# Kernel tuning notes

Hardware: AMD Instinct MI355X
Metric: run time of the kernel (lower is better)

Reference implementation:

```python
import jax, jax.numpy as jnp
import numpy as np

SQN = 3      # hardcoded recurrence depth
ATT_H = 256  # hardcoded attention hidden size
STRIDE = 16  # segment length (hardcoded expand(-1,16,-1))


def setup_inputs() -> dict:
    key = jax.random.key(0)
    ks = jax.random.split(key, 12)
    B, Cin, H, V = 64, 512, 512, 512

    def w(k, shape, fan_in):
        return jax.random.normal(k, shape, jnp.float32) / np.sqrt(fan_in).astype(np.float32)

    return {
        "visual_input": jax.random.normal(ks[0], (B, Cin, V), jnp.float32),
        "text_feature": jax.random.normal(ks[1], (B, H), jnp.float32),
        # weights stored [in, out] (transposed vs torch nn.Linear)
        "vis_conv_w": w(ks[2], (Cin, H), Cin),   # 1x1 Conv1d == linear over channels
        "vis_conv_b": jnp.zeros((H,), jnp.float32),
        "glob_w": w(ks[3], (SQN, H, H), H),      # 3 distinct global_emb linears
        "glob_b": jnp.zeros((SQN, H), jnp.float32),
        "guide_w": w(ks[4], (2 * H, H), 2 * H),
        "guide_b": jnp.zeros((H,), jnp.float32),
        "att1_w": w(ks[5], (H, ATT_H), H),
        "att1_b": jnp.zeros((ATT_H,), jnp.float32),
        "att2_w": w(ks[6], (H, ATT_H), H),
        "att2_b": jnp.zeros((ATT_H,), jnp.float32),
        "att3_w": w(ks[7], (ATT_H, 1), ATT_H),
        "att3_b": jnp.zeros((1,), jnp.float32),
        "out_conv_w": w(ks[8], (H, H), H),       # 1x1 Conv1d
        "out_conv_b": jnp.zeros((H,), jnp.float32),
        "text_w": w(ks[9], (H, H), H),
        "text_b": jnp.zeros((H,), jnp.float32),
    }


def reference(visual_input, text_feature, vis_conv_w, vis_conv_b, glob_w, glob_b,
              guide_w, guide_b, att1_w, att1_b, att2_w, att2_b, att3_w, att3_b,
              out_conv_w, out_conv_b, text_w, text_b):
    B, Cin, V = visual_input.shape
    H = vis_conv_w.shape[1]
    S = V // STRIDE  # number of segments

    # vis_conv (1x1) + relu: [B, H, V]
    vis_h = jax.nn.relu(jnp.einsum('bcv,ch->bhv', visual_input, vis_conv_w)
                        + vis_conv_b[None, :, None])
    # split into segments: [B, S, T=16, H]
    vis_seg = vis_h.reshape(B, H, S, STRIDE).transpose(0, 2, 3, 1)
    # AvgPool1d(kernel=stride) == per-segment mean: [B, S, H]
    avg_seg = vis_seg.mean(axis=2)
    # text projection: [B, H]
    text_att = text_feature @ text_w + text_b

    # precompute att_fn2(vis_seg): [B, S, T, ATT_H] (loop-invariant)
    att2_pre = jnp.einsum('bsth,ha->bsta', vis_seg, att2_w) + att2_b

    prev_se = jnp.zeros((B, S, H), vis_seg.dtype)
    se_list, att_list = [], []
    for m in range(SQN):  # fixed 3-step recurrence, distinct weights per step
        v_n = jnp.einsum('bsh,hk->bsk', avg_seg, glob_w[m]) + glob_b[m]
        # guide_emb (Linear+ReLU) followed by an outer relu == single relu
        g_n = jax.nn.relu(jnp.concatenate([v_n, prev_se], axis=-1) @ guide_w + guide_b)
        att = jnp.tanh((g_n @ att1_w + att1_b)[:, :, None, :] + att2_pre)  # [B,S,T,A]
        att = att @ att3_w + att3_b                                        # [B,S,T,1]
        att = jax.nn.softmax(att, axis=2)  # softmax over the 16 frames
        prev_se = jnp.sum(vis_seg * att, axis=2)  # [B, S, H]
        se_list.append(prev_se)
        att_list.append(att)

    vis_for_att = jnp.stack(se_list, axis=2)  # [B, S, 3, H]
    fuse_att = jax.nn.softmax(jnp.einsum('bsmh,bh->bsm', vis_for_att, text_att), axis=2)
    vis_new = jnp.einsum('bsmh,bsm->bsh', vis_for_att, fuse_att)  # [B, S, H]

    # vis_out_conv (1x1) + relu over stacked segments: [B, H, S]
    vis_out = jax.nn.relu(jnp.einsum('bsh,hk->bks', vis_new, out_conv_w)
                          + out_conv_b[None, :, None])
    att_out = jnp.concatenate(att_list, axis=3)  # [B, S, 16, 3]
    return vis_out, att_out
```

## Files before the change

### kernel.cpp

```cpp
#include <hip/hip_runtime.h>

#define B_   64
#define CIN_ 512
#define H_   512
#define V_   512
#define S_   32
#define T_   16
#define A_   256
#define SQN_ 3
#define BS_  2048

typedef float  f32x4  __attribute__((ext_vector_type(4)));
typedef float  f32x2  __attribute__((ext_vector_type(2)));
typedef short  short8 __attribute__((ext_vector_type(8)));
typedef short  short4v __attribute__((ext_vector_type(4)));
typedef unsigned int uint4v __attribute__((ext_vector_type(4)));

__device__ __forceinline__ unsigned short f2bf(float f) {
    union { float f; unsigned int u; } v; v.f = f;
    unsigned int u = v.u;
    unsigned int r = (u + 0x7fffu + ((u >> 16) & 1u)) >> 16;
    return (unsigned short)r;
}
__device__ __forceinline__ float bf2f(unsigned short h) {
    union { unsigned int u; float f; } v; v.u = ((unsigned int)h) << 16;
    return v.f;
}

__device__ __forceinline__ void gload16(const void* g, void* l) {
    __builtin_amdgcn_global_load_lds(
        (const __attribute__((address_space(1))) unsigned int*)g,
        (__attribute__((address_space(3))) unsigned int*)l,
        16, 0, 0);
}

__global__ __launch_bounds__(256) void prep_kernel(
    const float* __restrict__ visual, const float* __restrict__ vis_conv_w,
    const float* __restrict__ att2_w, const float* __restrict__ guide_w,
    const float* __restrict__ att1_w, const float* __restrict__ out_conv_w,
    const float* __restrict__ glob_w, const float* __restrict__ text_feature,
    const float* __restrict__ text_w, const float* __restrict__ text_b,
    const float* __restrict__ glob_b, const float* __restrict__ guide_b,
    unsigned short* __restrict__ visT, unsigned short* __restrict__ wT_visconv,
    unsigned short* __restrict__ wT_att2, unsigned short* __restrict__ wT_guide,
    unsigned short* __restrict__ wT_att1, unsigned short* __restrict__ wT_out,
    unsigned short* __restrict__ glob_bf, float* __restrict__ text_part,
    float* __restrict__ bcomb)
{
    __shared__ __align__(16) char smem[32768];
    const int id  = blockIdx.x;
    const int tid = threadIdx.x;

    if (id < 128) {
        const int nt = id & 7, kc = id >> 3;
        const int n0 = nt * 64, kbase = kc * 32;
        float* Ts = (float*)smem;
        float* Ws = (float*)smem + 64 * 33;
        {
            const int m = tid >> 2, kk = (tid & 3) * 8;
            #pragma unroll
            for (int c = 0; c < 8; c += 4)
                *(f32x4*)&Ts[m * 33 + kk + c] =
                    *(const f32x4*)&text_feature[m * 512 + kbase + kk + c];
            const int kr = tid >> 3, nn = (tid & 7) * 8;
            #pragma unroll
            for (int c = 0; c < 8; c += 4)
                *(f32x4*)&Ws[kr * 65 + nn + c] =
                    *(const f32x4*)&text_w[(long long)(kbase + kr) * 512 + n0 + nn + c];
        }
        __syncthreads();
        const int tm = (tid >> 4) * 4, tn = (tid & 15) * 4;
        float acc[4][4] = {};
        for (int k = 0; k < 32; k++) {
            float a[4], b2[4];
            #pragma unroll
            for (int i = 0; i < 4; i++) a[i] = Ts[(tm + i) * 33 + k];
            #pragma unroll
            for (int j = 0; j < 4; j++) b2[j] = Ws[k * 65 + tn + j];
            #pragma unroll
            for (int i = 0; i < 4; i++)
                #pragma unroll
                for (int j = 0; j < 4; j++) acc[i][j] += a[i] * b2[j];
        }
        #pragma unroll
        for (int i = 0; i < 4; i++)
            #pragma unroll
            for (int j = 0; j < 4; j++)
                text_part[kc * (64 * 512) + (tm + i) * 512 + n0 + tn + j] =
                    acc[i][j] + (kc == 0 ? text_b[n0 + tn + j] : 0.0f);
        return;
    }
    if (id < 131) {
        const int m = id - 128;
        const int j2 = tid * 2;
        float a0 = guide_b[j2], a1 = guide_b[j2 + 1];
        const float* gb = glob_b + m * 512;
        #pragma unroll 8
        for (int k = 0; k < 512; k++) {
            const float g = gb[k];
            f32x2 w = *(const f32x2*)&guide_w[(long long)k * 512 + j2];
            a0 += g * w[0];
            a1 += g * w[1];
        }
        f32x2 o = {a0, a1};
        *(f32x2*)&bcomb[m * 512 + j2] = o;
        return;
    }
    if (id < 227) {
        const int base = (id - 131) * 8192 + tid * 4;
        #pragma unroll
        for (int it = 0; it < 8; it++) {
            f32x4 v = *(const f32x4*)&glob_w[base + it * 1024];
            short4v o;
            #pragma unroll
            for (int c = 0; c < 4; c++) o[c] = (short)f2bf(v[c]);
            *(short4v*)&glob_bf[base + it * 1024] = o;
        }
        return;
    }

    if (id >= 547) {
        const int q = id - 547;
        const int b = q >> 5, tile = q & 31;
        const int k0 = (tile >> 2) << 6;
        const int v0 = (tile & 3) << 7;
        const float* src = visual + (long long)b * 262144;
        unsigned short* dst = visT + (long long)b * 262144;
        float* tl = (float*)smem;

        const int wave = tid >> 6, lane = tid & 63;
        #pragma unroll
        for (int i = 0; i < 8; i++) {
            const int r2 = wave * 16 + i * 2;
            gload16(&src[(long long)(k0 + r2 + (lane >> 5)) * 512 + v0 + (lane & 31) * 4],
                    &tl[r2 * 128]);
        }
        __syncthreads();

        const int kl = (tid & 7) * 8;
        const int vb = tid >> 3;
        #pragma unroll
        for (int jv = 0; jv < 4; jv++) {
            const int v = vb + jv * 32;
            short8 o;
            #pragma unroll
            for (int i = 0; i < 8; i++)
                o[i] = (short)f2bf(tl[(kl + i) * 128 + v]);
            *(short8*)&dst[(long long)(v0 + v) * 512 + k0 + kl] = o;
        }
        return;
    }

    const float* src; unsigned short* dst; int Kd, Nd, tile;
    if (id < 291)      { tile = id - 227; src = vis_conv_w; dst = wT_visconv; Kd = 512;  Nd = 512; }
    else if (id < 323) { tile = id - 291; src = att2_w;     dst = wT_att2;    Kd = 512;  Nd = 256; }
    else if (id < 451) { tile = id - 323; src = guide_w;    dst = wT_guide;   Kd = 1024; Nd = 512; }
    else if (id < 483) { tile = id - 451; src = att1_w;     dst = wT_att1;    Kd = 512;  Nd = 256; }
    else               { tile = id - 483; src = out_conv_w; dst = wT_out;     Kd = 512;  Nd = 512; }

    unsigned int* tl = (unsigned int*)smem;
    const int xw = Nd >> 6;
    const int n0 = (tile % xw) << 6, k0 = (tile / xw) << 6;
    {
        const int r = tid >> 4;
        const int c4 = (tid & 15) * 4;
        #pragma unroll
        for (int j = 0; j < 4; j++) {
            const int row = j * 16 + r;
            f32x4 v = *(const f32x4*)&src[(long long)(k0 + row) * Nd + n0 + c4];
            #pragma unroll
            for (int c2 = 0; c2 < 4; c2++)
                tl[row * 65 + c4 + c2] = f2bf(v[c2]);
        }
    }
    __syncthreads();
    {
        const int v = tid >> 2, cq = (tid & 3) * 16;
        short8 o0, o1;
        #pragma unroll
        for (int j = 0; j < 8; j++) o0[j] = (short)tl[(cq + j) * 65 + v];
        #pragma unroll
        for (int j = 0; j < 8; j++) o1[j] = (short)tl[(cq + 8 + j) * 65 + v];
        *(short8*)&dst[(long long)(n0 + v) * Kd + k0 + cq] = o0;
        *(short8*)&dst[(long long)(n0 + v) * Kd + k0 + cq + 8] = o1;
    }
}

template <int BM, int BN, bool RELU, bool OUT_BF16, int OUT_MODE, bool ACC_INIT>
__device__ __forceinline__ void gemm_body(
    char* pool, int bid, int nwg,
    const unsigned short* __restrict__ A, long long aBatch, int lda,
    const unsigned short* __restrict__ Bt, long long bBatch, int ldb,
    const float* __restrict__ bias, long long biasBatch,
    const float* __restrict__ Cinit, int ldci,
    void* __restrict__ C, long long cBatch, int ldc,
    void* __restrict__ C2, unsigned short* __restrict__ avg_out,
    int M, int N, int K)
{
    constexpr int WM = BM / 2, WN = BN / 2;
    constexpr int FI = WM / 16, FJ = WN / 16;
    constexpr bool CT_EN  = (OUT_MODE != 1);
    constexpr bool CT_F32 = CT_EN && ((OUT_MODE == 0 && !OUT_BF16) || OUT_MODE == 3);
    constexpr int  CTS    = CT_F32 ? (BN + 4) : (BN + 8);
    constexpr int  KLOOP_B = (2 * BM * 32 + 2 * BN * 32) * 2;
    constexpr int  CT_B    = CT_EN ? (BM * CTS * (CT_F32 ? 4 : 2)) : 0;
    constexpr int  MAIN_B  = (KLOOP_B > CT_B ? KLOOP_B : CT_B);
    unsigned short* As = (unsigned short*)pool;
    unsigned short* Bs = As + 2 * BM * 32;
    float* avgl = (float*)(pool + MAIN_B);

    const int q8 = nwg >> 3, r8 = nwg & 7;
    const int xcd = bid & 7, lid = bid >> 3;
    const int logical = (xcd < r8 ? xcd * (q8 + 1)
                                  : r8 * (q8 + 1) + (xcd - r8) * q8) + lid;

    const int ntiles = N / BN;
    const int tilesPerBatch = (M / BM) * ntiles;
    const int batch = logical / tilesPerBatch;
    const int t     = logical % tilesPerBatch;
    const int tm0 = (t / ntiles) * BM;
    const int tn0 = (t % ntiles) * BN;
    const unsigned short* Ab = A + (long long)batch * aBatch;
    const unsigned short* Bb = Bt + (long long)batch * bBatch;

    const int tid  = threadIdx.x;
    const int lane = tid & 63;
    const int wave = tid >> 6;
    const int wm = (wave >> 1) * WM;
    const int wn = (wave & 1) * WN;
    const int lr = lane & 15;
    const int lk = (lane >> 4) * 8;
    const int rsub = lane >> 2;
    const int g8   = (lane & 3) * 8;

    auto stage = [&](int buf, int k0) {
        #pragma unroll
        for (int i = 0; i < BM / 64; i++) {
            const int rbase = wave * (BM / 4) + i * 16;
            gload16(&Ab[(long long)(tm0 + rbase + rsub) * lda + k0 + g8],
                    &As[buf * (BM * 32) + rbase * 32]);
        }
        #pragma unroll
        for (int i = 0; i < BN / 64; i++) {
            const int rbase = wave * (BN / 4) + i * 16;
            gload16(&Bb[(long long)(tn0 + rbase + rsub) * ldb + k0 + g8],
                    &Bs[buf * (BN * 32) + rbase * 32]);
        }
    };

    f32x4 acc[FI][FJ] = {};
    const int nk = K >> 5;

    stage(0, 0);
    __syncthreads();
    int cur = 0;
    for (int kt = 0; kt < nk; kt++) {
        if (kt + 1 < nk) stage(cur ^ 1, (kt + 1) << 5);
        const unsigned short* Ac = As + cur * (BM * 32);
        const unsigned short* Bc = Bs + cur * (BN * 32);
        short8 a[FI], b[FJ];
        #pragma unroll
        for (int i = 0; i < FI; i++)
            a[i] = *(const short8*)&Ac[(wm + i * 16 + lr) * 32 + lk];
        #pragma unroll
        for (int j = 0; j < FJ; j++)
            b[j] = *(const short8*)&Bc[(wn + j * 16 + lr) * 32 + lk];
        #pragma unroll
        for (int i = 0; i < FI; i++)
            #pragma unroll
            for (int j = 0; j < FJ; j++)
                acc[i][j] = __builtin_amdgcn_mfma_f32_16x16x32_bf16(
                    a[i], b[j], acc[i][j], 0, 0, 0);
        if (kt + 1 < nk) { __syncthreads(); cur ^= 1; }
    }

    const int erow = (lane >> 4) * 4;
    const int ecol = lane & 15;

    if constexpr (OUT_MODE == 1) {
        #pragma unroll
        for (int i = 0; i < FI; i++) {
            #pragma unroll
            for (int j = 0; j < FJ; j++) {
                const int gcol = tn0 + wn + j * 16 + ecol;
                const float bv = bias ? bias[gcol] : 0.0f;
                const int grow0 = tm0 + wm + i * 16 + erow;
                const int bb = grow0 >> 5, ss = grow0 & 31;
                f32x4 o;
                #pragma unroll
                for (int r = 0; r < 4; r++) o[r] = fmaxf(acc[i][j][r] + bv, 0.0f);
                *(f32x4*)&((float*)C)[(long long)bb * (H_ * S_) + gcol * S_ + ss] = o;
            }
        }
        return;
    } else {
        __syncthreads();
        unsigned short* CTh = (unsigned short*)pool;
        float*          CTf = (float*)pool;

        #pragma unroll
        for (int i = 0; i < FI; i++) {
            #pragma unroll
            for (int j = 0; j < FJ; j++) {
                const int lcol = wn + j * 16 + ecol;
                const int gcol = tn0 + lcol;
                const float bv = bias ? bias[(long long)batch * biasBatch + gcol] : 0.0f;
                float csum = 0.0f;
                #pragma unroll
                for (int r = 0; r < 4; r++) {
                    const int lrow = wm + i * 16 + erow + r;
                    float v = acc[i][j][r] + bv;
                    if (ACC_INIT) v += Cinit[(long long)(tm0 + lrow) * ldci + gcol];
                    if (RELU) v = fmaxf(v, 0.0f);
                    if constexpr (CT_F32) CTf[lrow * CTS + lcol] = v;
                    else                  CTh[lrow * CTS + lcol] = f2bf(v);
                    if constexpr (OUT_MODE == 2) csum += v;
                }
                if constexpr (OUT_MODE == 2) {
                    csum += __shfl_xor(csum, 16, 64);
                    csum += __shfl_xor(csum, 32, 64);
                    if (lane < 16)
                        avgl[((wm >> 4) + i) * BN + wn + j * 16 + lane] = csum;
                }
            }
        }
        __syncthreads();

        if constexpr (CT_F32) {
            constexpr int ITERS = (BM * BN) / 1024;
            #pragma unroll
            for (int it = 0; it < ITERS; it++) {
                const int flat = it * 1024 + tid * 4;
                const int row = flat / BN, col = flat % BN;
                f32x4 vv = *(const f32x4*)&CTf[row * CTS + col];
                if constexpr (OUT_MODE == 3) {
                    if (batch == 0) {
                        short4v p;
                        #pragma unroll
                        for (int c = 0; c < 4; c++) p[c] = (short)f2bf(fmaxf(vv[c], 0.0f));
                        *(short4v*)&((unsigned short*)C2)[(long long)(tm0 + row) * ldc + tn0 + col] = p;
                    } else {
                        *(f32x4*)&((float*)C)[(long long)(batch - 1) * cBatch +
                                              (long long)(tm0 + row) * ldc + tn0 + col] = vv;
                    }
                } else {
                    *(f32x4*)&((float*)C)[(long long)batch * cBatch +
                                          (long long)(tm0 + row) * ldc + tn0 + col] = vv;
                }
            }
        } else {
            constexpr int ITERS = (BM * BN) / 2048;
            #pragma unroll
            for (int it = 0; it < ITERS; it++) {
                const int flat = it * 2048 + tid * 8;
                const int row = flat / BN, col = flat % BN;
                short8 vv = *(const short8*)&CTh[row * CTS + col];
                *(short8*)&((unsigned short*)C)[(long long)batch * cBatch +
                                                (long long)(tm0 + row) * ldc + tn0 + col] = vv;
            }
        }

        if constexpr (OUT_MODE == 2) {
            const int s = tid >> 5, hq = (tid & 31) * 4;
            short4v pk;
            #pragma unroll
            for (int c = 0; c < 4; c++)
                pk[c] = (short)f2bf(avgl[s * BN + hq + c] * (1.0f / 16.0f));
            *(short4v*)&avg_out[((long long)batch * 32 + (tm0 >> 4) + s) * H_ + tn0 + hq] = pk;
        }
    }
}

template <int BM, int BN, bool RELU, bool OUT_BF16, int OUT_MODE, bool ACC_INIT>
__global__ __launch_bounds__(256) void mfma_gemm(
    const unsigned short* A, long long aBatch, int lda,
    const unsigned short* Bt, long long bBatch, int ldb,
    const float* bias, long long biasBatch,
    const float* Cinit, int ldci,
    void* C, long long cBatch, int ldc,
    void* C2, unsigned short* avg_out,
    int M, int N, int K)
{
    constexpr bool CT_EN  = (OUT_MODE != 1);
    constexpr bool CT_F32 = CT_EN && ((OUT_MODE == 0 && !OUT_BF16) || OUT_MODE == 3);
    constexpr int  CTS    = CT_F32 ? (BN + 4) : (BN + 8);
    constexpr int  KLOOP_B = (2 * BM * 32 + 2 * BN * 32) * 2;
    constexpr int  CT_B    = CT_EN ? (BM * CTS * (CT_F32 ? 4 : 2)) : 0;
    constexpr int  MAIN_B  = (KLOOP_B > CT_B ? KLOOP_B : CT_B);
    constexpr int  AVG_B   = (OUT_MODE == 2) ? (BM / 16) * BN * 4 : 0;
    __shared__ __align__(16) char pool[MAIN_B + AVG_B];
    gemm_body<BM, BN, RELU, OUT_BF16, OUT_MODE, ACC_INIT>(
        pool, blockIdx.x, gridDim.x,
        A, aBatch, lda, Bt, bBatch, ldb, bias, biasBatch, Cinit, ldci,
        C, cBatch, ldc, C2, avg_out, M, N, K);
}

__global__ __launch_bounds__(256) void wcomb_visconv_kernel(
    const unsigned short* wT_guide, const unsigned short* glob_bf,
    unsigned short* WcombT,
    const unsigned short* visT, const unsigned short* wT_visconv,
    const float* vis_conv_b, unsigned short* vis_seg, unsigned short* avg)
{
    __shared__ __align__(16) char pool[40960];
    if (blockIdx.x < 192) {
        gemm_body<64, 64, false, true, 0, false>(pool, blockIdx.x, 192,
            wT_guide, 0, 1024,
            glob_bf, (long long)H_ * H_, H_,
            nullptr, 0, nullptr, 0,
            WcombT, (long long)H_ * H_, H_, nullptr, nullptr, H_, H_, H_);
    } else {
        gemm_body<128, 128, true, true, 2, false>(pool, blockIdx.x - 192, 1024,
            visT, (long long)V_ * CIN_, CIN_,
            wT_visconv, 0, CIN_,
            vis_conv_b, 0, nullptr, 0,
            vis_seg, (long long)V_ * H_, H_, nullptr, avg, V_, H_, CIN_);
    }
}

__global__ __launch_bounds__(256) void att2_p_kernel(
    const unsigned short* vis_seg, const unsigned short* wT_att2,
    const float* att2_b, unsigned short* att2_pre,
    const unsigned short* avg, const unsigned short* WcombT,
    const float* bcomb, float* P, unsigned short* gbuf)
{
    __shared__ __align__(16) char pool[40960];
    if (blockIdx.x < 512) {
        gemm_body<128, 128, false, true, 0, false>(pool, blockIdx.x, 512,
            vis_seg, (long long)V_ * H_, H_,
            wT_att2, 0, H_,
            att2_b, 0, nullptr, 0,
            att2_pre, (long long)V_ * A_, A_, nullptr, nullptr, V_, A_, H_);
    } else {
        gemm_body<64, 64, false, false, 3, false>(pool, blockIdx.x - 512, 768,
            avg, 0, H_,
            WcombT, (long long)H_ * H_, H_,
            bcomb, H_, nullptr, 0,
            P, (long long)BS_ * H_, H_, gbuf, nullptr, BS_, H_, H_);
    }
}

template <bool LAST>
__global__ __launch_bounds__(256) void fused_att_kernel(
    const float* __restrict__ att1,
    const unsigned short* __restrict__ att2_pre,
    const float* __restrict__ att3_w,
    const float* __restrict__ att3_b,
    const unsigned short* __restrict__ vis_seg,
    float* __restrict__ se_m,
    unsigned short* __restrict__ pse,
    float* __restrict__ att_out, int m,
    const float* __restrict__ se_base,
    const float* __restrict__ text_part,
    const float* __restrict__ text_b,
    unsigned short* __restrict__ vis_new)
{
    const int bs = blockIdx.x, tid = threadIdx.x;
    const int wave = tid >> 6, lane = tid & 63;
    __shared__ float logits[T_], wts[T_];
    __shared__ float part[3][512];
    __shared__ float redf[4][3];
    __shared__ float swf[3];
    __shared__ float tsh[512];

    if constexpr (LAST) {
        const int b = bs >> 5;
        for (int h = tid; h < 512; h += 256) {
            float s = text_b[h];
            #pragma unroll
            for (int p = 0; p < 16; p++)
                s += text_part[p * (64 * 512) + b * 512 + h];
            tsh[h] = s;
        }
    }

    f32x4 a1r = *(const f32x4*)&att1[(long long)bs * A_ + lane * 4];
    f32x4 w3r = *(const f32x4*)&att3_w[lane * 4];

    #pragma unroll
    for (int qq = 0; qq < 4; qq++) {
        const int t = wave * 4 + qq;
        short4v ap = *(const short4v*)&att2_pre[(long long)(bs * T_ + t) * A_ + lane * 4];
        float x = 0.f;
        #pragma unroll
        for (int c = 0; c < 4; c++)
            x += tanhf(a1r[c] + bf2f((unsigned short)ap[c])) * w3r[c];
        #pragma unroll
        for (int off = 32; off > 0; off >>= 1) x += __shfl_down(x, off, 64);
        if (lane == 0) logits[t] = x + att3_b[0];
    }
    __syncthreads();
    if (tid == 0) {
        float mx = logits[0];
        #pragma unroll
        for (int t = 1; t < T_; t++) mx = fmaxf(mx, logits[t]);
        float s = 0.f;
        #pragma unroll
        for (int t = 0; t < T_; t++) { float e = expf(logits[t] - mx); wts[t] = e; s += e; }
        float inv = 1.0f / s;
        #pragma unroll
        for (int t = 0; t < T_; t++) wts[t] *= inv;
    }
    __syncthreads();
    if (tid < T_) att_out[bs * (T_ * SQN_) + tid * SQN_ + m] = wts[tid];

    const int slot = tid & 63, quarter = tid >> 6;
    float s[8] = {};
    #pragma unroll
    for (int tt = 0; tt < 4; tt++) {
        const int t = quarter * 4 + tt;
        short8 vv = *(const short8*)&vis_seg[(long long)(bs * T_ + t) * H_ + slot * 8];
        const float w = wts[t];
        #pragma unroll
        for (int c = 0; c < 8; c++) s[c] += bf2f((unsigned short)vv[c]) * w;
    }
    if (quarter) {
        #pragma unroll
        for (int c = 0; c < 8; c++) part[quarter - 1][slot * 8 + c] = s[c];
    }
    __syncthreads();
    if (quarter == 0) {
        #pragma unroll
        for (int c = 0; c < 8; c++)
            s[c] += part[0][slot * 8 + c] + part[1][slot * 8 + c] + part[2][slot * 8 + c];
    }

    if constexpr (!LAST) {
        if (quarter == 0) {
            f32x4 o0 = {s[0], s[1], s[2], s[3]};
            f32x4 o1 = {s[4], s[5], s[6], s[7]};
            *(f32x4*)&se_m[(long long)bs * H_ + slot * 8] = o0;
            *(f32x4*)&se_m[(long long)bs * H_ + slot * 8 + 4] = o1;
            short8 p;
            #pragma unroll
            for (int c = 0; c < 8; c++) p[c] = (short)f2bf(s[c]);
            *(short8*)&pse[(long long)bs * H_ + slot * 8] = p;
        }
    } else {
        const float* se0 = se_base + (long long)bs * H_;
        const float* se1 = se_base + (long long)BS_ * H_ + (long long)bs * H_;

        float p0 = 0.f, p1 = 0.f, p2 = 0.f;
        {
            const int h2 = tid * 2;
            float t0 = tsh[h2], t1 = tsh[h2 + 1];
            p0 = se0[h2] * t0 + se0[h2 + 1] * t1;
            p1 = se1[h2] * t0 + se1[h2 + 1] * t1;
        }
        if (quarter == 0) {
            #pragma unroll
            for (int c = 0; c < 8; c++) p2 += s[c] * tsh[slot * 8 + c];
        }
        #pragma unroll
        for (int off = 32; off > 0; off >>= 1) {
            p0 += __shfl_down(p0, off, 64);
            p1 += __shfl_down(p1, off, 64);
            p2 += __shfl_down(p2, off, 64);
        }
        if (lane == 0) { redf[wave][0] = p0; redf[wave][1] = p1; redf[wave][2] = p2; }
        __syncthreads();
        if (tid == 0) {
            float d0 = redf[0][0] + redf[1][0] + redf[2][0] + redf[3][0];
            float d1 = redf[0][1] + redf[1][1] + redf[2][1] + redf[3][1];
            float d2 = redf[0][2] + redf[1][2] + redf[2][2] + redf[3][2];
            float mx = fmaxf(d0, fmaxf(d1, d2));
            float e0 = expf(d0 - mx), e1 = expf(d1 - mx), e2 = expf(d2 - mx);
            float inv = 1.0f / (e0 + e1 + e2);
            swf[0] = e0 * inv; swf[1] = e1 * inv; swf[2] = e2 * inv;
        }
        __syncthreads();
        if (quarter == 0) {
            const float w0 = swf[0], w1 = swf[1], w2 = swf[2];
            short8 p;
            #pragma unroll
            for (int c = 0; c < 8; c++) {
                const int h = slot * 8 + c;
                p[c] = (short)f2bf(w0 * se0[h] + w1 * se1[h] + w2 * s[c]);
            }
            *(short8*)&vis_new[(long long)bs * H_ + slot * 8] = p;
        }
    }
}

extern "C" void kernel_launch(void* const* d_in, const int* in_sizes, int n_in,
                              void* d_out, int out_size, void* d_ws, size_t ws_size,
                              hipStream_t stream)
{
    const float* visual       = (const float*)d_in[0];
    const float* text_feature = (const float*)d_in[1];
    const float* vis_conv_w   = (const float*)d_in[2];
    const float* vis_conv_b   = (const float*)d_in[3];
    const float* glob_w       = (const float*)d_in[4];
    const float* glob_b       = (const float*)d_in[5];
    const float* guide_w      = (const float*)d_in[6];
    const float* guide_b      = (const float*)d_in[7];
    const float* att1_w       = (const float*)d_in[8];
    const float* att1_b       = (const float*)d_in[9];
    const float* att2_w       = (const float*)d_in[10];
    const float* att2_b       = (const float*)d_in[11];
    const float* att3_w       = (const float*)d_in[12];
    const float* att3_b       = (const float*)d_in[13];
    const float* out_conv_w   = (const float*)d_in[14];
    const float* out_conv_b   = (const float*)d_in[15];
    const float* text_w       = (const float*)d_in[16];
    const float* text_b       = (const float*)d_in[17];
    float* out = (float*)d_out;
    float* att_out = out + (B_ * H_ * S_);

    char* base = (char*)d_ws;
    unsigned short* visT     = (unsigned short*)(base + 0);
    unsigned short* vis_seg  = (unsigned short*)(base + 33554432);
    unsigned short* att2_pre = (unsigned short*)(base + 67108864);
    float*          se       = (float*)(base + 100663296);
    float*          P        = (float*)(base + 113246208);
    unsigned short* pse      = (unsigned short*)(base + 125829120);
    unsigned short* gbuf     = (unsigned short*)(base + 127926272);
    float*          att1buf  = (float*)(base + 130023424);
    unsigned short* avg      = (unsigned short*)(base + 132120576);
    unsigned short* vis_new  = (unsigned short*)(base + 134348800);
    char*           wbase    = base + 136445952;
    unsigned short* wT_visconv = (unsigned short*)(wbase + 0);
    unsigned short* wT_att2    = (unsigned short*)(wbase + 524288);
    unsigned short* wT_guide   = (unsigned short*)(wbase + 786432);
    unsigned short* wT_att1    = (unsigned short*)(wbase + 1835008);
    unsigned short* wT_out     = (unsigned short*)(wbase + 2097152);
    unsigned short* glob_bf    = (unsigned short*)(wbase + 2621440);
    unsigned short* WcombT     = (unsigned short*)(wbase + 4194304);
    float*          bcomb      = (float*)(wbase + 5767168);
    float*          text_part  = (float*)(wbase + 6291456);

    prep_kernel<<<dim3(2595), 256, 0, stream>>>(
        visual, vis_conv_w, att2_w, guide_w, att1_w, out_conv_w, glob_w,
        text_feature, text_w, text_b, glob_b, guide_b,
        visT, wT_visconv, wT_att2, wT_guide, wT_att1, wT_out,
        glob_bf, text_part, bcomb);

    wcomb_visconv_kernel<<<dim3(192 + 1024), 256, 0, stream>>>(
        wT_guide, glob_bf, WcombT,
        visT, wT_visconv, vis_conv_b, vis_seg, avg);

    att2_p_kernel<<<dim3(512 + 768), 256, 0, stream>>>(
        vis_seg, wT_att2, att2_b, att2_pre,
        avg, WcombT, bcomb, P, gbuf);

    for (int m = 0; m < SQN_; m++) {
        if (m > 0) {
            mfma_gemm<64, 64, true, true, 0, true><<<dim3(256), 256, 0, stream>>>(
                pse, 0, H_,
                wT_guide + 512, 0, 1024,
                nullptr, 0, P + (long long)(m - 1) * BS_ * H_, H_,
                gbuf, 0, H_, nullptr, nullptr, BS_, H_, H_);
        }
        mfma_gemm<64, 64, false, false, 0, false><<<dim3(128), 256, 0, stream>>>(
            gbuf, 0, H_,
            wT_att1, 0, H_,
            att1_b, 0, nullptr, 0,
            att1buf, 0, A_, nullptr, nullptr, BS_, A_, H_);
        if (m < SQN_ - 1) {
            fused_att_kernel<false><<<dim3(BS_), 256, 0, stream>>>(
                att1buf, att2_pre, att3_w, att3_b, vis_seg,
                se + (long long)m * BS_ * H_, pse, att_out, m,
                nullptr, nullptr, nullptr, nullptr);
        } else {
            fused_att_kernel<true><<<dim3(BS_), 256, 0, stream>>>(
                att1buf, att2_pre, att3_w, att3_b, vis_seg,
                nullptr, nullptr, att_out, m,
                se, text_part, text_b, vis_new);
        }
    }

    mfma_gemm<64, 64, true, false, 1, false><<<dim3(256), 256, 0, stream>>>(
        vis_new, 0, H_,
        wT_out, 0, H_,
        out_conv_b, 0, nullptr, 0,
        out, 0, 0, nullptr, nullptr, BS_, H_, H_);
}
```

Measured before the change: 184.1 us.

## Split fused wcomb/visconv launch and use dedicated 256x256-tile visconv GEMM kernel

Replaces the combined wcomb+visconv launch with two launches: a plain mfma_gemm for the Wcomb weight product, and a new 512-thread visconv kernel using 256x256 tiles with a 128KB double-buffered LDS, swizzled loads, setprio around MFMA bursts, and a fused bias/ReLU/segment-average epilogue. Larger tiles are meant to raise data reuse and MFMA density for the dominant vis_conv GEMM. In exchange it adds an extra kernel launch, drops the overlap between the two GEMMs, and uses only 256 blocks, which may underfill the GPU's CUs.

```diff
diff --git a/kernel.cpp b/kernel.cpp
--- a/kernel.cpp
+++ b/kernel.cpp
@@ -395,25 +395,153 @@
         C, cBatch, ldc, C2, avg_out, M, N, K);
 }
 
-__global__ __launch_bounds__(256) void wcomb_visconv_kernel(
-    const unsigned short* wT_guide, const unsigned short* glob_bf,
-    unsigned short* WcombT,
-    const unsigned short* visT, const unsigned short* wT_visconv,
-    const float* vis_conv_b, unsigned short* vis_seg, unsigned short* avg)
+__global__ __launch_bounds__(512, 2) void visconv256_kernel(
+    const unsigned short* __restrict__ A,
+    const unsigned short* __restrict__ Bw,
+    const float* __restrict__ bias,
+    unsigned short* __restrict__ Cseg,
+    unsigned short* __restrict__ avg_out)
 {
-    __shared__ __align__(16) char pool[40960];
-    if (blockIdx.x < 192) {
-        gemm_body<64, 64, false, true, 0, false>(pool, blockIdx.x, 192,
-            wT_guide, 0, 1024,
-            glob_bf, (long long)H_ * H_, H_,
-            nullptr, 0, nullptr, 0,
-            WcombT, (long long)H_ * H_, H_, nullptr, nullptr, H_, H_, H_);
-    } else {
-        gemm_body<128, 128, true, true, 2, false>(pool, blockIdx.x - 192, 1024,
-            visT, (long long)V_ * CIN_, CIN_,
-            wT_visconv, 0, CIN_,
-            vis_conv_b, 0, nullptr, 0,
-            vis_seg, (long long)V_ * H_, H_, nullptr, avg, V_, H_, CIN_);
+    __shared__ __align__(16) char pool[131072];
+    const int tid  = threadIdx.x;
+    const int wave = tid >> 6, lane = tid & 63;
+
+    const int bid     = blockIdx.x;
+    const int logical = (bid & 7) * 32 + (bid >> 3);
+    const int b   = logical >> 2;
+    const int tm0 = ((logical >> 1) & 1) * 256;
+    const int tn0 = (logical & 1) * 256;
+
+    const unsigned short* Ab = A + (long long)b * ((long long)V_ * CIN_);
+
+    const int fo   = wave * 1024 + lane * 16;
+    const int lo   = fo ^ (((fo >> 9) & 1) << 5);
+    const int srow = lo >> 6;
+    const int skel = (lo & 63) >> 1;
+
+    const int wr = wave >> 2;
+    const int hb = (wave >> 1) & 1;
+    const int lr = lane & 15;
+    const int kofs  = ((lane >> 4) * 16) ^ ((lane & 8) ? 32 : 0);
+    const int abase = wr * 16384 + lr * 64 + kofs;
+    const int bbase = hb * 16384 + ((wave & 1) * 64 + lr) * 64 + kofs;
+
+    auto stage = [&](int t) {
+        char* dstb = pool + (t & 1) * 65536;
+        const int k0 = t << 6;
+        #pragma unroll
+        for (int c = 0; c < 4; c++) {
+            gload16(&Ab[(long long)(tm0 + (c >> 1) * 128 + srow) * 512
+                        + k0 + (c & 1) * 32 + skel],
+                    dstb + c * 8192 + wave * 1024);
+            gload16(&Bw[(long long)(tn0 + (c >> 1) * 128 + srow) * 512
+                        + k0 + (c & 1) * 32 + skel],
+                    dstb + 32768 + c * 8192 + wave * 1024);
+        }
+    };
+
+    f32x4 acc[8][4] = {};
+
+    stage(0);
+    asm volatile("s_waitcnt vmcnt(0)" ::: "memory");
+    __builtin_amdgcn_s_barrier();
+
+    #pragma unroll
+    for (int t = 0; t < 8; t++) {
+        const char* Abuf = pool + (t & 1) * 65536;
+        const char* Bbuf = Abuf + 32768;
+        short8 bfr[4][2], afr[2][2];
+
+        #pragma unroll
+        for (int j = 0; j < 4; j++)
+            #pragma unroll
+            for (int ks = 0; ks < 2; ks++)
+                bfr[j][ks] = *(const short8*)(Bbuf + bbase + ks * 8192 + j * 1024);
+        #pragma unroll
+        for (int ii = 0; ii < 2; ii++)
+            #pragma unroll
+            for (int ks = 0; ks < 2; ks++)
+                afr[ii][ks] = *(const short8*)(Abuf + abase + ks * 8192 + ii * 1024);
+        if (t < 7) stage(t + 1);
+        __builtin_amdgcn_s_barrier();
+        __builtin_amdgcn_s_setprio(1);
+        #pragma unroll
+        for (int ks = 0; ks < 2; ks++)
+            #pragma unroll
+            for (int ii = 0; ii < 2; ii++)
+                #pragma unroll
+                for (int j = 0; j < 4; j++)
+                    acc[ii][j] = __builtin_amdgcn_mfma_f32_16x16x32_bf16(
+                        afr[ii][ks], bfr[j][ks], acc[ii][j], 0, 0, 0);
+        __builtin_amdgcn_s_setprio(0);
+        __builtin_amdgcn_s_barrier();
+
+        #pragma unroll
+        for (int p = 1; p < 4; p++) {
+            #pragma unroll
+            for (int ii = 0; ii < 2; ii++)
+                #pragma unroll
+                for (int ks = 0; ks < 2; ks++)
+                    afr[ii][ks] = *(const short8*)(Abuf + abase + ks * 8192
+                                                   + (p * 2 + ii) * 1024);
+            __builtin_amdgcn_s_barrier();
+            __builtin_amdgcn_s_setprio(1);
+            #pragma unroll
+            for (int ks = 0; ks < 2; ks++)
+                #pragma unroll
+                for (int ii = 0; ii < 2; ii++)
+                    #pragma unroll
+                    for (int j = 0; j < 4; j++)
+                        acc[p * 2 + ii][j] = __builtin_amdgcn_mfma_f32_16x16x32_bf16(
+                            afr[ii][ks], bfr[j][ks], acc[p * 2 + ii][j], 0, 0, 0);
+            __builtin_amdgcn_s_setprio(0);
+            if (p == 3) asm volatile("s_waitcnt vmcnt(0)" ::: "memory");
+            __builtin_amdgcn_s_barrier();
+        }
+    }
+
+    const int erow = (lane >> 4) * 4;
+    const int ecol = lane & 15;
+    const int wn   = (wave & 3) * 64;
+    unsigned short* CT = (unsigned short*)pool;
+    __syncthreads();
+
+    float bv[4];
+    #pragma unroll
+    for (int j = 0; j < 4; j++) bv[j] = bias[tn0 + wn + j * 16 + ecol];
+
+    #pragma unroll
+    for (int half = 0; half < 2; half++) {
+        if (wr == half) {
+            #pragma unroll
+            for (int i = 0; i < 8; i++) {
+                #pragma unroll
+                for (int j = 0; j < 4; j++) {
+                    float csum = 0.0f;
+                    #pragma unroll
+                    for (int r = 0; r < 4; r++) {
+                        float v = fmaxf(acc[i][j][r] + bv[j], 0.0f);
+                        CT[(i * 16 + erow + r) * 264 + wn + j * 16 + ecol] = f2bf(v);
+                        csum += v;
+                    }
+                    csum += __shfl_xor(csum, 16, 64);
+                    csum += __shfl_xor(csum, 32, 64);
+                    if (lane < 16)
+                        avg_out[((long long)b * 32 + (tm0 >> 4) + half * 8 + i) * H_
+                                + tn0 + wn + j * 16 + lane] = f2bf(csum * (1.0f / 16.0f));
+                }
+            }
+        }
+        __syncthreads();
+        #pragma unroll
+        for (int it = 0; it < 8; it++) {
+            const int flat = it * 4096 + tid * 8;
+            const int row = flat >> 8, col = flat & 255;
+            short8 vv = *(const short8*)&CT[row * 264 + col];
+            *(short8*)&Cseg[(long long)(b * 512 + tm0 + half * 128 + row) * 512
+                            + tn0 + col] = vv;
+        }
+        __syncthreads();
     }
 }
 
@@ -634,8 +762,13 @@
         visT, wT_visconv, wT_att2, wT_guide, wT_att1, wT_out,
         glob_bf, text_part, bcomb);
 
-    wcomb_visconv_kernel<<<dim3(192 + 1024), 256, 0, stream>>>(
-        wT_guide, glob_bf, WcombT,
+    mfma_gemm<64, 64, false, true, 0, false><<<dim3(192), 256, 0, stream>>>(
+        wT_guide, 0, 1024,
+        glob_bf, (long long)H_ * H_, H_,
+        nullptr, 0, nullptr, 0,
+        WcombT, (long long)H_ * H_, H_, nullptr, nullptr, H_, H_, H_);
+
+    visconv256_kernel<<<dim3(256), 512, 0, stream>>>(
         visT, wT_visconv, vis_conv_b, vis_seg, avg);
 
     att2_p_kernel<<<dim3(512 + 768), 256, 0, stream>>>(
```

Measured after the change: 210.9 us. +14.6%, slower.

## Add multi-stage LDS pipeline with swizzle, explicit vmcnt waits, and fast tanh

Applied to the files above, without the earlier changes.

Makes the GEMM k-loop depth configurable, using triple buffering for the small recurrence GEMMs. The full __syncthreads is replaced by explicit s_waitcnt vmcnt counts plus raw barriers, so later tiles' async global->LDS loads can stay in flight. An XOR swizzle is applied to the LDS column offsets to reduce bank conflicts on the short8 reads. tanhf in the attention kernel is replaced by an exp/rcp approximation, which costs some precision.

```diff
diff --git a/kernel.cpp b/kernel.cpp
--- a/kernel.cpp
+++ b/kernel.cpp
@@ -27,11 +27,21 @@
     return v.f;
 }
 
+__device__ __forceinline__ float fast_tanhf(float x) {
+    float cx = fminf(fmaxf(x, -15.0f), 15.0f);
+    float e  = __expf(2.0f * cx);
+    return (e - 1.0f) * __builtin_amdgcn_rcpf(e + 1.0f);
+}
+
 __device__ __forceinline__ void gload16(const void* g, void* l) {
     __builtin_amdgcn_global_load_lds(
         (const __attribute__((address_space(1))) unsigned int*)g,
         (__attribute__((address_space(3))) unsigned int*)l,
         16, 0, 0);
+}
+
+template <int N> __device__ __forceinline__ void waitv() {
+    asm volatile("s_waitcnt vmcnt(%0)" :: "n"(N) : "memory");
 }
 
 __global__ __launch_bounds__(256) void prep_kernel(
@@ -186,7 +196,7 @@
     }
 }
 
-template <int BM, int BN, bool RELU, bool OUT_BF16, int OUT_MODE, bool ACC_INIT>
+template <int BM, int BN, bool RELU, bool OUT_BF16, int OUT_MODE, bool ACC_INIT, int DEPTH>
 __device__ __forceinline__ void gemm_body(
     char* pool, int bid, int nwg,
     const unsigned short* __restrict__ A, long long aBatch, int lda,
@@ -199,14 +209,15 @@
 {
     constexpr int WM = BM / 2, WN = BN / 2;
     constexpr int FI = WM / 16, FJ = WN / 16;
+    constexpr int LOADS = BM / 64 + BN / 64;
     constexpr bool CT_EN  = (OUT_MODE != 1);
     constexpr bool CT_F32 = CT_EN && ((OUT_MODE == 0 && !OUT_BF16) || OUT_MODE == 3);
     constexpr int  CTS    = CT_F32 ? (BN + 4) : (BN + 8);
-    constexpr int  KLOOP_B = (2 * BM * 32 + 2 * BN * 32) * 2;
+    constexpr int  KLOOP_B = DEPTH * (BM * 32 + BN * 32) * 2;
     constexpr int  CT_B    = CT_EN ? (BM * CTS * (CT_F32 ? 4 : 2)) : 0;
     constexpr int  MAIN_B  = (KLOOP_B > CT_B ? KLOOP_B : CT_B);
     unsigned short* As = (unsigned short*)pool;
-    unsigned short* Bs = As + 2 * BM * 32;
+    unsigned short* Bs = As + DEPTH * BM * 32;
     float* avgl = (float*)(pool + MAIN_B);
 
     const int q8 = nwg >> 3, r8 = nwg & 7;
@@ -231,19 +242,20 @@
     const int lr = lane & 15;
     const int lk = (lane >> 4) * 8;
     const int rsub = lane >> 2;
-    const int g8   = (lane & 3) * 8;
+    const int g8s = ((lane & 3) ^ ((lane >> 3) & 3)) * 8;
+    const int lks = lk ^ (((lr >> 1) & 3) << 3);
 
     auto stage = [&](int buf, int k0) {
         #pragma unroll
         for (int i = 0; i < BM / 64; i++) {
             const int rbase = wave * (BM / 4) + i * 16;
-            gload16(&Ab[(long long)(tm0 + rbase + rsub) * lda + k0 + g8],
+            gload16(&Ab[(long long)(tm0 + rbase + rsub) * lda + k0 + g8s],
                     &As[buf * (BM * 32) + rbase * 32]);
         }
         #pragma unroll
         for (int i = 0; i < BN / 64; i++) {
             const int rbase = wave * (BN / 4) + i * 16;
-            gload16(&Bb[(long long)(tn0 + rbase + rsub) * ldb + k0 + g8],
+            gload16(&Bb[(long long)(tn0 + rbase + rsub) * ldb + k0 + g8s],
                     &Bs[buf * (BN * 32) + rbase * 32]);
         }
     };
@@ -251,27 +263,43 @@
     f32x4 acc[FI][FJ] = {};
     const int nk = K >> 5;
 
-    stage(0, 0);
-    __syncthreads();
+    #pragma unroll
+    for (int d = 0; d < DEPTH - 1; d++)
+        if (d < nk) stage(d, d << 5);
+
     int cur = 0;
     for (int kt = 0; kt < nk; kt++) {
-        if (kt + 1 < nk) stage(cur ^ 1, (kt + 1) << 5);
+        if (kt + DEPTH - 1 < nk) {
+            const int nb = cur + DEPTH - 1;
+            stage(nb >= DEPTH ? nb - DEPTH : nb, (kt + DEPTH - 1) << 5);
+        }
+        if constexpr (DEPTH == 2) {
+            if (kt + 1 < nk) waitv<LOADS>(); else waitv<0>();
+        } else {
+            if (kt + 2 < nk)      waitv<2 * LOADS>();
+            else if (kt + 1 < nk) waitv<LOADS>();
+            else                  waitv<0>();
+        }
+        __builtin_amdgcn_s_barrier();
+
         const unsigned short* Ac = As + cur * (BM * 32);
         const unsigned short* Bc = Bs + cur * (BN * 32);
         short8 a[FI], b[FJ];
         #pragma unroll
         for (int i = 0; i < FI; i++)
-            a[i] = *(const short8*)&Ac[(wm + i * 16 + lr) * 32 + lk];
+            a[i] = *(const short8*)&Ac[(wm + i * 16 + lr) * 32 + lks];
         #pragma unroll
         for (int j = 0; j < FJ; j++)
-            b[j] = *(const short8*)&Bc[(wn + j * 16 + lr) * 32 + lk];
+            b[j] = *(const short8*)&Bc[(wn + j * 16 + lr) * 32 + lks];
         #pragma unroll
         for (int i = 0; i < FI; i++)
             #pragma unroll
             for (int j = 0; j < FJ; j++)
                 acc[i][j] = __builtin_amdgcn_mfma_f32_16x16x32_bf16(
                     a[i], b[j], acc[i][j], 0, 0, 0);
-        if (kt + 1 < nk) { __syncthreads(); cur ^= 1; }
+        __builtin_amdgcn_sched_barrier(0);
+        __builtin_amdgcn_s_barrier();
+        cur = (cur + 1 == DEPTH) ? 0 : cur + 1;
     }
 
     const int erow = (lane >> 4) * 4;
@@ -371,7 +399,7 @@
     }
 }
 
-template <int BM, int BN, bool RELU, bool OUT_BF16, int OUT_MODE, bool ACC_INIT>
+template <int BM, int BN, bool RELU, bool OUT_BF16, int OUT_MODE, bool ACC_INIT, int DEPTH>
 __global__ __launch_bounds__(256) void mfma_gemm(
     const unsigned short* A, long long aBatch, int lda,
     const unsigned short* Bt, long long bBatch, int ldb,
@@ -384,12 +412,12 @@
     constexpr bool CT_EN  = (OUT_MODE != 1);
     constexpr bool CT_F32 = CT_EN && ((OUT_MODE == 0 && !OUT_BF16) || OUT_MODE == 3);
     constexpr int  CTS    = CT_F32 ? (BN + 4) : (BN + 8);
-    constexpr int  KLOOP_B = (2 * BM * 32 + 2 * BN * 32) * 2;
+    constexpr int  KLOOP_B = DEPTH * (BM * 32 + BN * 32) * 2;
     constexpr int  CT_B    = CT_EN ? (BM * CTS * (CT_F32 ? 4 : 2)) : 0;
     constexpr int  MAIN_B  = (KLOOP_B > CT_B ? KLOOP_B : CT_B);
     constexpr int  AVG_B   = (OUT_MODE == 2) ? (BM / 16) * BN * 4 : 0;
     __shared__ __align__(16) char pool[MAIN_B + AVG_B];
-    gemm_body<BM, BN, RELU, OUT_BF16, OUT_MODE, ACC_INIT>(
+    gemm_body<BM, BN, RELU, OUT_BF16, OUT_MODE, ACC_INIT, DEPTH>(
         pool, blockIdx.x, gridDim.x,
         A, aBatch, lda, Bt, bBatch, ldb, bias, biasBatch, Cinit, ldci,
         C, cBatch, ldc, C2, avg_out, M, N, K);
@@ -401,15 +429,15 @@
     const unsigned short* visT, const unsigned short* wT_visconv,
     const float* vis_conv_b, unsigned short* vis_seg, unsigned short* avg)
 {
-    __shared__ __align__(16) char pool[40960];
+    __shared__ __align__(16) char pool[38912];
     if (blockIdx.x < 192) {
-        gemm_body<64, 64, false, true, 0, false>(pool, blockIdx.x, 192,
+        gemm_body<64, 64, false, true, 0, false, 2>(pool, blockIdx.x, 192,
             wT_guide, 0, 1024,
             glob_bf, (long long)H_ * H_, H_,
             nullptr, 0, nullptr, 0,
             WcombT, (long long)H_ * H_, H_, nullptr, nullptr, H_, H_, H_);
     } else {
-        gemm_body<128, 128, true, true, 2, false>(pool, blockIdx.x - 192, 1024,
+        gemm_body<128, 128, true, true, 2, false, 2>(pool, blockIdx.x - 192, 1024,
             visT, (long long)V_ * CIN_, CIN_,
             wT_visconv, 0, CIN_,
             vis_conv_b, 0, nullptr, 0,
@@ -423,15 +451,15 @@
     const unsigned short* avg, const unsigned short* WcombT,
     const float* bcomb, float* P, unsigned short* gbuf)
 {
-    __shared__ __align__(16) char pool[40960];
+    __shared__ __align__(16) char pool[34816];
     if (blockIdx.x < 512) {
-        gemm_body<128, 128, false, true, 0, false>(pool, blockIdx.x, 512,
+        gemm_body<128, 128, false, true, 0, false, 2>(pool, blockIdx.x, 512,
             vis_seg, (long long)V_ * H_, H_,
             wT_att2, 0, H_,
             att2_b, 0, nullptr, 0,
             att2_pre, (long long)V_ * A_, A_, nullptr, nullptr, V_, A_, H_);
     } else {
-        gemm_body<64, 64, false, false, 3, false>(pool, blockIdx.x - 512, 768,
+        gemm_body<64, 64, false, false, 3, false, 2>(pool, blockIdx.x - 512, 768,
             avg, 0, H_,
             WcombT, (long long)H_ * H_, H_,
             bcomb, H_, nullptr, 0,
@@ -483,7 +511,7 @@
         float x = 0.f;
         #pragma unroll
         for (int c = 0; c < 4; c++)
-            x += tanhf(a1r[c] + bf2f((unsigned short)ap[c])) * w3r[c];
+            x += fast_tanhf(a1r[c] + bf2f((unsigned short)ap[c])) * w3r[c];
         #pragma unroll
         for (int off = 32; off > 0; off >>= 1) x += __shfl_down(x, off, 64);
         if (lane == 0) logits[t] = x + att3_b[0];
@@ -644,13 +672,13 @@
 
     for (int m = 0; m < SQN_; m++) {
         if (m > 0) {
-            mfma_gemm<64, 64, true, true, 0, true><<<dim3(256), 256, 0, stream>>>(
+            mfma_gemm<64, 64, true, true, 0, true, 3><<<dim3(256), 256, 0, stream>>>(
                 pse, 0, H_,
                 wT_guide + 512, 0, 1024,
                 nullptr, 0, P + (long long)(m - 1) * BS_ * H_, H_,
                 gbuf, 0, H_, nullptr, nullptr, BS_, H_, H_);
         }
-        mfma_gemm<64, 64, false, false, 0, false><<<dim3(128), 256, 0, stream>>>(
+        mfma_gemm<64, 64, false, false, 0, false, 3><<<dim3(128), 256, 0, stream>>>(
             gbuf, 0, H_,
             wT_att1, 0, H_,
             att1_b, 0, nullptr, 0,
@@ -668,7 +696,7 @@
         }
     }
 
-    mfma_gemm<64, 64, true, false, 1, false><<<dim3(256), 256, 0, stream>>>(
+    mfma_gemm<64, 64, true, false, 1, false, 3><<<dim3(256), 256, 0, stream>>>(
         vis_new, 0, H_,
         wT_out, 0, H_,
         out_conv_b, 0, nullptr, 0,
```

Measured after the change: 165.9 us. 9.9% less time.
